# Performance work log

Hardware: AMD Instinct MI355X
Metric: run time of the kernel (lower is better)

The kernel has to match this reference:

```python
import jax, jax.numpy as jnp
import numpy as np

B, SX, TY = 256, 180, 160
D, DK, DV, H, DFF, V = 512, 64, 64, 8, 2048, 30
EPS = 1e-5


def _ln(x, g, b):
    m = jnp.mean(x, axis=-1, keepdims=True)
    v = jnp.mean(jnp.square(x - m), axis=-1, keepdims=True)
    return (x - m) / jnp.sqrt(v + EPS) * g + b


def _mha(q, kv, wq, wk, wv, pw, pb, masked):
    # per-head projections, vectorized over heads (source loops in Python)
    C = q.shape[-1]  # scale uses d_model (input dim), faithful to source
    Q = jnp.einsum('btd,hdk->bhtk', q, wq)
    K = jnp.einsum('bsd,hdk->bhsk', kv, wk)
    Vv = jnp.einsum('bsd,hdv->bhsv', kv, wv)
    W = jnp.einsum('bhtk,bhsk->bhts', Q, K) / (C ** 0.5)
    if masked:
        T = q.shape[1]
        tri = jnp.tril(jnp.ones((T, T), dtype=bool))
        W = jnp.where(tri, W, -jnp.inf)
    W = jax.nn.softmax(W, axis=-1)  # dropout is identity at rate 0 / eval
    out = jnp.einsum('bhts,bhsv->bthv', W, Vv)
    out = out.reshape(q.shape[0], q.shape[1], -1)  # concat heads -> [B,T,H*DV]
    return out @ pw + pb


def _attn_block(q, kv, wq, wk, wv, pw, pb, g, b, masked):
    res = q + _mha(q, kv, wq, wk, wv, pw, pb, masked)
    return _ln(res, g, b)


def _ff_block(x, w1, b1, w2, b2, g, b):
    h = jax.nn.relu(x @ w1 + b1) @ w2 + b2
    return _ln(x + h, g, b)


def setup_inputs() -> dict:
    key = jax.random.key(0)
    ks = iter(jax.random.split(key, 64))

    def n(shape, s=0.05):
        return jax.random.normal(next(ks), shape, jnp.float32) * s

    inp = {}
    inp['x'] = jax.random.normal(next(ks), (B, SX, 2), jnp.float32)
    inp['targets'] = jax.random.randint(next(ks), (B, TY + 1), 0, V, jnp.int32)
    inp['spec_w'] = n((2, D), 0.5)
    inp['spec_b'] = jnp.zeros((D,), jnp.float32)
    inp['pep_emb'] = n((V, D), 0.5)
    for p in ['enc_at', 'dec_sat', 'dec_cat']:
        inp[p + '_wq'] = n((H, D, DK))
        inp[p + '_wk'] = n((H, D, DK))
        inp[p + '_wv'] = n((H, D, DV))
        inp[p + '_pw'] = n((H * DV, D))
        inp[p + '_pb'] = jnp.zeros((D,), jnp.float32)
        inp[p + '_g'] = jnp.ones((D,), jnp.float32)
        inp[p + '_b'] = jnp.zeros((D,), jnp.float32)
    for p in ['enc_ff', 'dec_ff']:
        inp[p + '_w1'] = n((D, DFF))
        inp[p + '_b1'] = jnp.zeros((DFF,), jnp.float32)
        inp[p + '_w2'] = n((DFF, D))
        inp[p + '_b2'] = jnp.zeros((D,), jnp.float32)
        inp[p + '_g'] = jnp.ones((D,), jnp.float32)
        inp[p + '_b'] = jnp.zeros((D,), jnp.float32)
    inp['ll_w'] = n((D, V))
    inp['ll_b'] = jnp.zeros((V,), jnp.float32)
    return inp


def reference(x, targets, spec_w, spec_b, pep_emb,
              enc_at_wq, enc_at_wk, enc_at_wv, enc_at_pw, enc_at_pb, enc_at_g, enc_at_b,
              dec_sat_wq, dec_sat_wk, dec_sat_wv, dec_sat_pw, dec_sat_pb, dec_sat_g, dec_sat_b,
              dec_cat_wq, dec_cat_wk, dec_cat_wv, dec_cat_pw, dec_cat_pb, dec_cat_g, dec_cat_b,
              enc_ff_w1, enc_ff_b1, enc_ff_w2, enc_ff_b2, enc_ff_g, enc_ff_b,
              dec_ff_w1, dec_ff_b1, dec_ff_w2, dec_ff_b2, dec_ff_g, dec_ff_b,
              ll_w, ll_b):
    tgt = targets[:, :-1]
    xe = x @ spec_w + spec_b                      # spectrum embedding [B,SX,D]
    enc = _attn_block(xe, xe, enc_at_wq, enc_at_wk, enc_at_wv, enc_at_pw, enc_at_pb, enc_at_g, enc_at_b, False)
    enc = _ff_block(enc, enc_ff_w1, enc_ff_b1, enc_ff_w2, enc_ff_b2, enc_ff_g, enc_ff_b)
    de = pep_emb[tgt]                             # peptide embedding [B,TY,D]
    d1 = _attn_block(de, de, dec_sat_wq, dec_sat_wk, dec_sat_wv, dec_sat_pw, dec_sat_pb, dec_sat_g, dec_sat_b, True)
    d2 = _attn_block(d1, enc, dec_cat_wq, dec_cat_wk, dec_cat_wv, dec_cat_pw, dec_cat_pb, dec_cat_g, dec_cat_b, False)
    d3 = _ff_block(d2, dec_ff_w1, dec_ff_b1, dec_ff_w2, dec_ff_b2, dec_ff_g, dec_ff_b)
    return d3 @ ll_w + ll_b                       # logits [B,TY,V]
```

## Files before the change

### kernel.cpp

```cpp
#include <hip/hip_runtime.h>
#include <hip/hip_bf16.h>

typedef __hip_bfloat16 bf16;
typedef __attribute__((ext_vector_type(8))) short short8;
typedef __attribute__((ext_vector_type(4))) float f32x4;

#define BB   256
#define SXX  180
#define TYY  160
#define DD   512
#define DKK  64
#define HH   8
#define DFFF 2048
#define VV   30

#define NE (BB * SXX)
#define ND (BB * TYY)
#define N_IN 40

#ifndef __has_builtin
#define __has_builtin(x) 0
#endif

__global__ void k_detect(const unsigned short* __restrict__ probe, int* __restrict__ flag)
{
    if (threadIdx.x == 0 && blockIdx.x == 0)
        *flag = (probe[0] != 0x3F80) ? 1 : 0;
}

__device__ __forceinline__ float ldin(const void* src, long i, int f32)
{
    return f32 ? ((const float*)src)[i] : __bfloat162float(((const bf16*)src)[i]);
}

struct ImpD { const void* src; bf16* dst; int n; int K; int N; int mode; int blk0; int pad; };
struct ImpT { ImpD d[N_IN]; };

__global__ __launch_bounds__(256) void k_import_all(ImpT t, const int* __restrict__ flag)
{
    const int bid = blockIdx.x;
    int which = 0;
    #pragma unroll
    for (int k = 1; k < N_IN; ++k)
        if (bid >= t.d[k].blk0) which = k;
    ImpD d = t.d[which];
    if (d.mode == 3) return;
    long li = (long)(bid - d.blk0) * 256 + threadIdx.x;
    if (li >= d.n) return;
    int f32 = *flag;
    float v;
    if (d.mode == 0) {
        v = ldin(d.src, li, f32);
    } else if (d.mode == 1) {
        int nrow = (int)(li / d.K);
        int k    = (int)(li - (long)nrow * d.K);
        v = (nrow < d.N) ? ldin(d.src, (long)k * d.N + nrow, f32) : 0.f;
    } else {
        int n1 = (int)(li >> 9), dd = (int)(li & 511);
        v = ldin(d.src, (long)(n1 >> 6) * (DD * DKK) + (long)dd * DKK + (n1 & 63), f32);
    }
    d.dst[li] = __float2bfloat16(v);
}

__global__ __launch_bounds__(256) void k_embed_spec(
    const bf16* __restrict__ x, const bf16* __restrict__ w,
    const bf16* __restrict__ b, bf16* __restrict__ out)
{
    long i = (long)blockIdx.x * 256 + threadIdx.x;
    if (i >= (long)NE * DD) return;
    long tok = i >> 9;
    int  d   = (int)(i & 511);
    float x0 = __bfloat162float(x[tok * 2 + 0]);
    float x1 = __bfloat162float(x[tok * 2 + 1]);
    out[i] = __float2bfloat16(x0 * __bfloat162float(w[d])
                            + x1 * __bfloat162float(w[DD + d])
                            + __bfloat162float(b[d]));
}

__global__ __launch_bounds__(256) void k_gather(
    const int* __restrict__ tg, const bf16* __restrict__ emb, bf16* __restrict__ out)
{
    long tok = blockIdx.x;
    int  b   = (int)(tok / TYY);
    int  t   = (int)(tok - (long)b * TYY);
    int  idx = tg[(long)b * (TYY + 1) + t];
    const bf16* src = emb + (long)idx * DD;
    bf16*       dst = out + tok * DD;
    dst[threadIdx.x]       = src[threadIdx.x];
    dst[threadIdx.x + 256] = src[threadIdx.x + 256];
}

__device__ __forceinline__ void stage16(const bf16* g, bf16* l)
{
#if __has_builtin(__builtin_amdgcn_global_load_lds)
    __builtin_amdgcn_global_load_lds(
        (const __attribute__((address_space(1))) unsigned int*)g,
        (__attribute__((address_space(3))) unsigned int*)l, 16, 0, 0);
#else
    *(short8*)l = *(const short8*)g;
#endif
}

__global__ __launch_bounds__(256, 1) void k_mgemm(
    const bf16* __restrict__ A, const bf16* __restrict__ BT,
    const bf16* __restrict__ bias, const bf16* __restrict__ res,
    void* __restrict__ C,
    int M, int N, int K, int lda, int ldb, int ldc,
    int relu, const int* __restrict__ outf32)
{
    __shared__ __align__(16) bf16 sh[8192];
    bf16* As = sh;
    bf16* Bs = sh + 4096;

    const int tid  = threadIdx.x;
    const int lane = tid & 63;
    const int w    = tid >> 6;
    const int m0   = blockIdx.y * 128;
    const int n0   = blockIdx.x * 128;
    const int mw   = (w >> 1) * 64;
    const int nw   = (w & 1) * 64;

    f32x4 acc[4][4];
    #pragma unroll
    for (int i = 0; i < 4; ++i)
        #pragma unroll
        for (int j = 0; j < 4; ++j)
            acc[i][j] = (f32x4){0.f, 0.f, 0.f, 0.f};

    const int  sr = tid >> 2;
    const int  sk = (tid & 3) * 8;
    const bf16* Ag0 = A  + (size_t)(m0 + sr) * lda + sk;
    const bf16* Ag1 = Ag0 + (size_t)64 * lda;
    const bf16* Bg0 = BT + (size_t)(n0 + sr) * ldb + sk;
    const bf16* Bg1 = Bg0 + (size_t)64 * ldb;
    bf16* Al0 = As + sr * 32 + sk;
    bf16* Al1 = Al0 + 64 * 32;
    bf16* Bl0 = Bs + sr * 32 + sk;
    bf16* Bl1 = Bl0 + 64 * 32;

    const int lc = lane & 15, lq = lane >> 4;

    for (int k0 = 0; k0 < K; k0 += 32) {
        stage16(Ag0 + k0, Al0);
        stage16(Ag1 + k0, Al1);
        stage16(Bg0 + k0, Bl0);
        stage16(Bg1 + k0, Bl1);
        __syncthreads();

        short8 af[4], bfr[4];
        #pragma unroll
        for (int i = 0; i < 4; ++i)
            af[i] = *(const short8*)(As + (mw + i * 16 + lc) * 32 + lq * 8);
        #pragma unroll
        for (int j = 0; j < 4; ++j)
            bfr[j] = *(const short8*)(Bs + (nw + j * 16 + lc) * 32 + lq * 8);

        #pragma unroll
        for (int i = 0; i < 4; ++i)
            #pragma unroll
            for (int j = 0; j < 4; ++j)
                acc[i][j] = __builtin_amdgcn_mfma_f32_16x16x32_bf16(
                    af[i], bfr[j], acc[i][j], 0, 0, 0);

        __syncthreads();
    }

    const int f32o = (outf32 != nullptr) ? *outf32 : 0;

    if (!f32o && (N & 127) == 0) {
        float bv[4];
        #pragma unroll
        for (int j = 0; j < 4; ++j)
            bv[j] = bias ? __bfloat162float(bias[n0 + nw + j * 16 + lc]) : 0.f;
        bf16* ep = sh;
        #pragma unroll
        for (int i = 0; i < 4; ++i) {
            __syncthreads();
            #pragma unroll
            for (int j = 0; j < 4; ++j)
                #pragma unroll
                for (int r = 0; r < 4; ++r) {
                    float v = acc[i][j][r] + bv[j];
                    if (relu && v < 0.f) v = 0.f;
                    int lr = (w >> 1) * 16 + lq * 4 + r;
                    ep[lr * 136 + nw + j * 16 + lc] = __float2bfloat16(v);
                }
            __syncthreads();
            #pragma unroll
            for (int u = 0; u < 2; ++u) {
                int slot = tid + 256 * u;
                int lr   = slot >> 4;
                int cb   = (slot & 15) << 3;
                int gm   = m0 + 16 * i + ((lr & 16) ? (48 + lr) : lr);
                int gn   = n0 + cb;
                short8 val = *(short8*)(ep + lr * 136 + cb);
                if (res) {
                    short8 rv = *(const short8*)(res + (size_t)gm * ldc + gn);
                    #pragma unroll
                    for (int e = 0; e < 8; ++e) {
                        float s = __bfloat162float(((bf16*)&val)[e])
                                + __bfloat162float(((bf16*)&rv)[e]);
                        ((bf16*)&val)[e] = __float2bfloat16(s);
                    }
                }
                *(short8*)((bf16*)C + (size_t)gm * ldc + gn) = val;
            }
        }
    } else {
        #pragma unroll
        for (int j = 0; j < 4; ++j) {
            int gn = n0 + nw + j * 16 + lc;
            if (gn >= N) continue;
            float bvj = bias ? __bfloat162float(bias[gn]) : 0.f;
            #pragma unroll
            for (int i = 0; i < 4; ++i) {
                int gm = m0 + mw + i * 16 + lq * 4;
                #pragma unroll
                for (int r = 0; r < 4; ++r) {
                    float v = acc[i][j][r] + bvj;
                    if (relu && v < 0.f) v = 0.f;
                    size_t off = (size_t)(gm + r) * ldc + gn;
                    if (res) v += __bfloat162float(res[off]);
                    if (f32o) ((float*)C)[off] = v;
                    else      ((bf16*)C)[off]  = __float2bfloat16(v);
                }
            }
        }
    }
}

__global__ __launch_bounds__(256, 1) void k_fattn(
    const bf16* __restrict__ Q, const bf16* __restrict__ Kc,
    const bf16* __restrict__ Vt, bf16* __restrict__ O,
    int T, int S, int b_off, int causal, int ldv)
{
    __shared__ __align__(16) bf16 Pl[4 * 48 * 72];
    const int bl = blockIdx.x, h = blockIdx.y;
    const int tid = threadIdx.x, lane = tid & 63, w = tid >> 6;
    const int lc = lane & 15, lq = lane >> 4;
    const int wr0 = w * 48;
    const float scl = 0.044194173824159216f;

    short8 Qf[3][2];
    #pragma unroll
    for (int i = 0; i < 3; ++i) {
        int t = wr0 + 16 * i + lc;
        if (t >= T) t = T - 1;
        const bf16* qp = Q + ((size_t)(bl + b_off) * T + t) * DD + h * 64;
        #pragma unroll
        for (int kt = 0; kt < 2; ++kt)
            Qf[i][kt] = *(const short8*)(qp + kt * 32 + lq * 8);
    }

    float mrow[3][4], lrow[3][4];
    f32x4 oacc[3][4];
    #pragma unroll
    for (int i = 0; i < 3; ++i)
        #pragma unroll
        for (int r = 0; r < 4; ++r) { mrow[i][r] = -1e30f; lrow[i][r] = 0.f; }
    #pragma unroll
    for (int i = 0; i < 3; ++i)
        #pragma unroll
        for (int n = 0; n < 4; ++n)
            oacc[i][n] = (f32x4){0.f, 0.f, 0.f, 0.f};

    bf16* pw = Pl + w * 48 * 72;

    for (int c0 = 0; c0 < 192; c0 += 64) {
        if (causal && c0 > wr0 + 47) continue;

        short8 Kf[4][2];
        #pragma unroll
        for (int j = 0; j < 4; ++j) {
            int s = c0 + 16 * j + lc;
            if (s >= S) s = S - 1;
            const bf16* kp = Kc + ((size_t)bl * S + s) * DD + h * 64;
            #pragma unroll
            for (int kt = 0; kt < 2; ++kt)
                Kf[j][kt] = *(const short8*)(kp + kt * 32 + lq * 8);
        }

        f32x4 sa[3][4];
        #pragma unroll
        for (int i = 0; i < 3; ++i)
            #pragma unroll
            for (int j = 0; j < 4; ++j)
                sa[i][j] = (f32x4){0.f, 0.f, 0.f, 0.f};
        #pragma unroll
        for (int i = 0; i < 3; ++i)
            #pragma unroll
            for (int j = 0; j < 4; ++j)
                #pragma unroll
                for (int kt = 0; kt < 2; ++kt)
                    sa[i][j] = __builtin_amdgcn_mfma_f32_16x16x32_bf16(
                        Qf[i][kt], Kf[j][kt], sa[i][j], 0, 0, 0);

        #pragma unroll
        for (int i = 0; i < 3; ++i)
            #pragma unroll
            for (int j = 0; j < 4; ++j) {
                int col = c0 + 16 * j + lc;
                #pragma unroll
                for (int r = 0; r < 4; ++r) {
                    int row = wr0 + 16 * i + lq * 4 + r;
                    float v = sa[i][j][r] * scl;
                    if (col >= S || (causal && col > row)) v = -1e30f;
                    sa[i][j][r] = v;
                }
            }

        float corr[3][4];
        #pragma unroll
        for (int i = 0; i < 3; ++i)
            #pragma unroll
            for (int r = 0; r < 4; ++r) {
                float cm = fmaxf(fmaxf(sa[i][0][r], sa[i][1][r]),
                                 fmaxf(sa[i][2][r], sa[i][3][r]));
                cm = fmaxf(cm, __shfl_xor(cm, 1));
                cm = fmaxf(cm, __shfl_xor(cm, 2));
                cm = fmaxf(cm, __shfl_xor(cm, 4));
                cm = fmaxf(cm, __shfl_xor(cm, 8));
                float mn = fmaxf(mrow[i][r], cm);
                corr[i][r] = __expf(mrow[i][r] - mn);
                mrow[i][r] = mn;
            }
        #pragma unroll
        for (int i = 0; i < 3; ++i)
            #pragma unroll
            for (int j = 0; j < 4; ++j)
                #pragma unroll
                for (int r = 0; r < 4; ++r)
                    sa[i][j][r] = __expf(sa[i][j][r] - mrow[i][r]);
        #pragma unroll
        for (int i = 0; i < 3; ++i)
            #pragma unroll
            for (int r = 0; r < 4; ++r) {
                float sm = sa[i][0][r] + sa[i][1][r] + sa[i][2][r] + sa[i][3][r];
                sm += __shfl_xor(sm, 1);
                sm += __shfl_xor(sm, 2);
                sm += __shfl_xor(sm, 4);
                sm += __shfl_xor(sm, 8);
                lrow[i][r] = lrow[i][r] * corr[i][r] + sm;
            }

        #pragma unroll
        for (int i = 0; i < 3; ++i)
            #pragma unroll
            for (int j = 0; j < 4; ++j)
                #pragma unroll
                for (int r = 0; r < 4; ++r)
                    pw[(16 * i + lq * 4 + r) * 72 + 16 * j + lc] =
                        __float2bfloat16(sa[i][j][r]);

        short8 Pf[3][2], Vf[4][2];
        #pragma unroll
        for (int i = 0; i < 3; ++i)
            #pragma unroll
            for (int kt = 0; kt < 2; ++kt)
                Pf[i][kt] = *(const short8*)(pw + (16 * i + lc) * 72 + kt * 32 + lq * 8);
        #pragma unroll
        for (int n = 0; n < 4; ++n)
            #pragma unroll
            for (int kt = 0; kt < 2; ++kt)
                Vf[n][kt] = *(const short8*)(Vt + (size_t)(h * 64 + 16 * n + lc) * ldv
                                             + (size_t)bl * S + c0 + kt * 32 + lq * 8);

        #pragma unroll
        for (int i = 0; i < 3; ++i)
            #pragma unroll
            for (int n = 0; n < 4; ++n) {
                #pragma unroll
                for (int r = 0; r < 4; ++r)
                    oacc[i][n][r] *= corr[i][r];
                #pragma unroll
                for (int kt = 0; kt < 2; ++kt)
                    oacc[i][n] = __builtin_amdgcn_mfma_f32_16x16x32_bf16(
                        Pf[i][kt], Vf[n][kt], oacc[i][n], 0, 0, 0);
            }
    }

    #pragma unroll
    for (int i = 0; i < 3; ++i)
        #pragma unroll
        for (int r = 0; r < 4; ++r) {
            int t = wr0 + 16 * i + lq * 4 + r;
            if (t >= T) continue;
            float inv = 1.f / lrow[i][r];
            bf16* op = O + ((size_t)(bl + b_off) * T + t) * DD + h * 64;
            #pragma unroll
            for (int n = 0; n < 4; ++n)
                op[16 * n + lc] = __float2bfloat16(oacc[i][n][r] * inv);
        }
}

__global__ __launch_bounds__(256) void k_ln(
    const bf16* __restrict__ in, const bf16* __restrict__ g,
    const bf16* __restrict__ b, bf16* __restrict__ out)
{
    __shared__ float red[256];
    long long base = (long long)blockIdx.x * DD;
    int tid = threadIdx.x;
    float v0 = __bfloat162float(in[base + tid]);
    float v1 = __bfloat162float(in[base + 256 + tid]);

    red[tid] = v0 + v1; __syncthreads();
    for (int st = 128; st > 0; st >>= 1) {
        if (tid < st) red[tid] += red[tid + st];
        __syncthreads();
    }
    float mean = red[0] * (1.f / DD);
    __syncthreads();

    float d0 = v0 - mean, d1 = v1 - mean;
    red[tid] = d0 * d0 + d1 * d1; __syncthreads();
    for (int st = 128; st > 0; st >>= 1) {
        if (tid < st) red[tid] += red[tid + st];
        __syncthreads();
    }
    float rstd = rsqrtf(red[0] * (1.f / DD) + 1e-5f);

    out[base + tid] = __float2bfloat16(d0 * rstd * __bfloat162float(g[tid])
                                       + __bfloat162float(b[tid]));
    out[base + 256 + tid] = __float2bfloat16(d1 * rstd * __bfloat162float(g[tid + 256])
                                             + __bfloat162float(b[tid + 256]));
}

static inline void mgemm(hipStream_t s, const bf16* A, const bf16* BT, const bf16* bias,
                         const bf16* res, void* C, int M, int N, int K,
                         int lda, int ldb, int ldc, int relu, const int* outf32 = nullptr)
{
    dim3 grid((N + 127) / 128, M / 128);
    k_mgemm<<<grid, dim3(256), 0, s>>>(A, BT, bias, res, C, M, N, K, lda, ldb, ldc,
                                       relu, outf32);
}

extern "C" void kernel_launch(void* const* d_in, const int* in_sizes, int n_in,
                              void* d_out, int out_size, void* d_ws, size_t ws_size,
                              hipStream_t stream)
{
    char* base = (char*)d_ws;
    size_t o = 0;
    auto take = [&](size_t bytes) { size_t r = o; o += (bytes + 255) & ~(size_t)255; return r; };

    int* dflag = (int*)(base + take(256));
    k_detect<<<dim3(1), dim3(64), 0, stream>>>((const unsigned short*)d_in[10], dflag);

    ImpT tab;
    int blk = 0;
    const bf16* cv[N_IN];
    auto add_imp = [&](int i, int mode, int K, int N, int n_elems) {
        bf16* dst = (bf16*)(base + take((size_t)n_elems * 2));
        tab.d[i] = ImpD{d_in[i], dst, n_elems, K, N, mode, blk, 0};
        blk += (n_elems + 255) / 256;
        cv[i] = dst;
    };
    for (int i = 0; i < N_IN; ++i) {
        if (i == 1) { tab.d[i] = ImpD{nullptr, nullptr, 0, 0, 0, 3, blk, 0}; cv[i] = nullptr; continue; }
        bool qkv = (i == 5 || i == 6 || i == 7 || i == 12 || i == 13 || i == 14 ||
                    i == 19 || i == 20 || i == 21);
        if (qkv)                        add_imp(i, 2, 0, 0, DD * DD);
        else if (i == 8 || i == 15 || i == 22) add_imp(i, 1, DD, DD, DD * DD);
        else if (i == 26 || i == 32)    add_imp(i, 1, DD, DFFF, DFFF * DD);
        else if (i == 28 || i == 34)    add_imp(i, 1, DFFF, DD, DD * DFFF);
        else if (i == 38)               add_imp(i, 1, DD, VV, 128 * DD);
        else                            add_imp(i, 0, 0, 0, in_sizes[i]);
    }
    k_import_all<<<dim3(blk), dim3(256), 0, stream>>>(tab, dflag);

    const int* targets = (const int*)d_in[1];
    const bf16 *x = cv[0], *spec_w = cv[2], *spec_b = cv[3], *pep_emb = cv[4];
    const bf16 *eat_wq = cv[5],  *eat_wk = cv[6],  *eat_wvT = cv[7],  *eat_pw = cv[8],
               *eat_pb = cv[9],  *eat_g  = cv[10], *eat_b   = cv[11];
    const bf16 *sat_wq = cv[12], *sat_wk = cv[13], *sat_wvT = cv[14], *sat_pw = cv[15],
               *sat_pb = cv[16], *sat_g  = cv[17], *sat_b   = cv[18];
    const bf16 *cat_wq = cv[19], *cat_wk = cv[20], *cat_wvT = cv[21], *cat_pw = cv[22],
               *cat_pb = cv[23], *cat_g  = cv[24], *cat_b   = cv[25];
    const bf16 *eff_w1 = cv[26], *eff_b1 = cv[27], *eff_w2 = cv[28], *eff_b2 = cv[29],
               *eff_g  = cv[30], *eff_b  = cv[31];
    const bf16 *dff_w1 = cv[32], *dff_b1 = cv[33], *dff_w2 = cv[34], *dff_b2 = cv[35],
               *dff_g  = cv[36], *dff_b  = cv[37];
    const bf16 *ll_w = cv[38], *ll_b = cv[39];

    const size_t REG = (size_t)NE * DD * 2;
    bf16* A = (bf16*)(base + take(REG));
    bf16* B = (bf16*)(base + take(REG));
    bf16* C = (bf16*)(base + take(REG));
    bf16* D = (bf16*)(base + take(REG + 4096));
    bf16* D2 = D + (size_t)(NE / 2) * DD;

    k_embed_spec<<<dim3((NE * DD + 255) / 256), dim3(256), 0, stream>>>(x, spec_w, spec_b, A);

    mgemm(stream, A, eat_wq, nullptr, nullptr, B, NE, DD, DD, DD, DD, DD, 0);
    for (int hb = 0; hb < 2; ++hb) {
        const bf16* kv = A + (size_t)hb * (NE / 2) * DD;
        mgemm(stream, kv, eat_wk, nullptr, nullptr, D, NE / 2, DD, DD, DD, DD, DD, 0);
        mgemm(stream, eat_wvT, kv, nullptr, nullptr, D2, DD, NE / 2, DD, DD, DD, NE / 2, 0);
        k_fattn<<<dim3(BB / 2, HH), dim3(256), 0, stream>>>(
            B, D, D2, B, SXX, SXX, hb * (BB / 2), 0, NE / 2);
    }
    mgemm(stream, B, eat_pw, eat_pb, A, C, NE, DD, DD, DD, DD, DD, 0);
    k_ln<<<dim3(NE), dim3(256), 0, stream>>>(C, eat_g, eat_b, A);

    {
        const int CH = NE / 4;
        for (int c = 0; c < 4; ++c) {
            const bf16* Ain = A + (size_t)c * CH * DD;
            mgemm(stream, Ain, eff_w1, eff_b1, nullptr, B, CH, DFFF, DD, DD, DD, DFFF, 1);
            mgemm(stream, B, eff_w2, eff_b2, Ain, C + (size_t)c * CH * DD,
                  CH, DD, DFFF, DFFF, DFFF, DD, 0);
        }
        k_ln<<<dim3(NE), dim3(256), 0, stream>>>(C, eff_g, eff_b, C);
    }

    k_gather<<<dim3(ND), dim3(256), 0, stream>>>(targets, pep_emb, A);

    mgemm(stream, A, sat_wq, nullptr, nullptr, B, ND, DD, DD, DD, DD, DD, 0);
    for (int hb = 0; hb < 2; ++hb) {
        const bf16* kv = A + (size_t)hb * (ND / 2) * DD;
        mgemm(stream, kv, sat_wk, nullptr, nullptr, D, ND / 2, DD, DD, DD, DD, DD, 0);
        mgemm(stream, sat_wvT, kv, nullptr, nullptr, D2, DD, ND / 2, DD, DD, DD, ND / 2, 0);
        k_fattn<<<dim3(BB / 2, HH), dim3(256), 0, stream>>>(
            B, D, D2, B, TYY, TYY, hb * (BB / 2), 1, ND / 2);
    }
    mgemm(stream, B, sat_pw, sat_pb, A, D, ND, DD, DD, DD, DD, DD, 0);
    k_ln<<<dim3(ND), dim3(256), 0, stream>>>(D, sat_g, sat_b, A);

    mgemm(stream, A, cat_wq, nullptr, nullptr, B, ND, DD, DD, DD, DD, DD, 0);
    for (int hb = 0; hb < 2; ++hb) {
        const bf16* kv = C + (size_t)hb * (NE / 2) * DD;
        mgemm(stream, kv, cat_wk, nullptr, nullptr, D, NE / 2, DD, DD, DD, DD, DD, 0);
        mgemm(stream, cat_wvT, kv, nullptr, nullptr, D2, DD, NE / 2, DD, DD, DD, NE / 2, 0);
        k_fattn<<<dim3(BB / 2, HH), dim3(256), 0, stream>>>(
            B, D, D2, B, TYY, SXX, hb * (BB / 2), 0, NE / 2);
    }
    mgemm(stream, B, cat_pw, cat_pb, A, D, ND, DD, DD, DD, DD, DD, 0);
    k_ln<<<dim3(ND), dim3(256), 0, stream>>>(D, cat_g, cat_b, A);

    {
        const int CH = ND / 4;
        for (int c = 0; c < 4; ++c) {
            const bf16* Ain = A + (size_t)c * CH * DD;
            mgemm(stream, Ain, dff_w1, dff_b1, nullptr, B, CH, DFFF, DD, DD, DD, DFFF, 1);
            mgemm(stream, B, dff_w2, dff_b2, Ain, D + (size_t)c * CH * DD,
                  CH, DD, DFFF, DFFF, DFFF, DD, 0);
        }
        k_ln<<<dim3(ND), dim3(256), 0, stream>>>(D, dff_g, dff_b, D);
    }

    mgemm(stream, D, ll_w, ll_b, nullptr, d_out, ND, VV, DD, DD, DD, VV, 0, dflag);

    (void)in_sizes; (void)n_in; (void)out_size; (void)ws_size;
}
```

Baseline: 2.058 ms.

## Double-buffer GEMM LDS tiles and halve FFN chunk count

The GEMM main loop now keeps two LDS buffers. It prefetches the next K-slice with global_load_lds while MFMAs consume the current one, which drops one barrier per iteration. This targets the exposed global-load latency of the single-buffered loop, at the cost of doubling LDS to 32 KB per block. The FFN stages now run in two chunks instead of four, giving larger and fewer GEMM launches. To make room, the FFN hidden buffer is allowed to spill from B into the adjacent C region, and the attention scratch buffers are reassigned to match.

```diff
diff --git a/kernel.cpp b/kernel.cpp
--- a/kernel.cpp
+++ b/kernel.cpp
@@ -108,9 +108,7 @@
     int M, int N, int K, int lda, int ldb, int ldc,
     int relu, const int* __restrict__ outf32)
 {
-    __shared__ __align__(16) bf16 sh[8192];
-    bf16* As = sh;
-    bf16* Bs = sh + 4096;
+    __shared__ __align__(16) bf16 sh[16384];
 
     const int tid  = threadIdx.x;
     const int lane = tid & 63;
@@ -133,27 +131,33 @@
     const bf16* Ag1 = Ag0 + (size_t)64 * lda;
     const bf16* Bg0 = BT + (size_t)(n0 + sr) * ldb + sk;
     const bf16* Bg1 = Bg0 + (size_t)64 * ldb;
-    bf16* Al0 = As + sr * 32 + sk;
-    bf16* Al1 = Al0 + 64 * 32;
-    bf16* Bl0 = Bs + sr * 32 + sk;
-    bf16* Bl1 = Bl0 + 64 * 32;
+    const int lofs = sr * 32 + sk;
 
     const int lc = lane & 15, lq = lane >> 4;
 
+    stage16(Ag0, sh + lofs);
+    stage16(Ag1, sh + 2048 + lofs);
+    stage16(Bg0, sh + 4096 + lofs);
+    stage16(Bg1, sh + 6144 + lofs);
+
     for (int k0 = 0; k0 < K; k0 += 32) {
-        stage16(Ag0 + k0, Al0);
-        stage16(Ag1 + k0, Al1);
-        stage16(Bg0 + k0, Bl0);
-        stage16(Bg1 + k0, Bl1);
+        bf16* cb = sh + ((k0 >> 5) & 1) * 8192;
         __syncthreads();
+        if (k0 + 32 < K) {
+            bf16* nb = sh + ((~(k0 >> 5)) & 1) * 8192;
+            stage16(Ag0 + k0 + 32, nb + lofs);
+            stage16(Ag1 + k0 + 32, nb + 2048 + lofs);
+            stage16(Bg0 + k0 + 32, nb + 4096 + lofs);
+            stage16(Bg1 + k0 + 32, nb + 6144 + lofs);
+        }
 
         short8 af[4], bfr[4];
         #pragma unroll
         for (int i = 0; i < 4; ++i)
-            af[i] = *(const short8*)(As + (mw + i * 16 + lc) * 32 + lq * 8);
+            af[i] = *(const short8*)(cb + (mw + i * 16 + lc) * 32 + lq * 8);
         #pragma unroll
         for (int j = 0; j < 4; ++j)
-            bfr[j] = *(const short8*)(Bs + (nw + j * 16 + lc) * 32 + lq * 8);
+            bfr[j] = *(const short8*)(cb + 4096 + (nw + j * 16 + lc) * 32 + lq * 8);
 
         #pragma unroll
         for (int i = 0; i < 4; ++i)
@@ -161,8 +165,6 @@
             for (int j = 0; j < 4; ++j)
                 acc[i][j] = __builtin_amdgcn_mfma_f32_16x16x32_bf16(
                     af[i], bfr[j], acc[i][j], 0, 0, 0);
-
-        __syncthreads();
     }
 
     const int f32o = (outf32 != nullptr) ? *outf32 : 0;
@@ -190,10 +192,10 @@
             for (int u = 0; u < 2; ++u) {
                 int slot = tid + 256 * u;
                 int lr   = slot >> 4;
-                int cb   = (slot & 15) << 3;
+                int cb2  = (slot & 15) << 3;
                 int gm   = m0 + 16 * i + ((lr & 16) ? (48 + lr) : lr);
-                int gn   = n0 + cb;
-                short8 val = *(short8*)(ep + lr * 136 + cb);
+                int gn   = n0 + cb2;
+                short8 val = *(short8*)(ep + lr * 136 + cb2);
                 if (res) {
                     short8 rv = *(const short8*)(res + (size_t)gm * ldc + gn);
                     #pragma unroll
@@ -486,7 +488,8 @@
     bf16* B = (bf16*)(base + take(REG));
     bf16* C = (bf16*)(base + take(REG));
     bf16* D = (bf16*)(base + take(REG + 4096));
-    bf16* D2 = D + (size_t)(NE / 2) * DD;
+    bf16* D2  = D + (size_t)(NE / 2) * DD;
+    bf16* H   = B;
 
     k_embed_spec<<<dim3((NE * DD + 255) / 256), dim3(256), 0, stream>>>(x, spec_w, spec_b, A);
 
@@ -502,46 +505,48 @@
     k_ln<<<dim3(NE), dim3(256), 0, stream>>>(C, eat_g, eat_b, A);
 
     {
-        const int CH = NE / 4;
-        for (int c = 0; c < 4; ++c) {
+        const int CH = NE / 2;
+        for (int c = 0; c < 2; ++c) {
             const bf16* Ain = A + (size_t)c * CH * DD;
-            mgemm(stream, Ain, eff_w1, eff_b1, nullptr, B, CH, DFFF, DD, DD, DD, DFFF, 1);
-            mgemm(stream, B, eff_w2, eff_b2, Ain, C + (size_t)c * CH * DD,
+            mgemm(stream, Ain, eff_w1, eff_b1, nullptr, H, CH, DFFF, DD, DD, DD, DFFF, 1);
+            mgemm(stream, H, eff_w2, eff_b2, Ain, D + (size_t)c * CH * DD,
                   CH, DD, DFFF, DFFF, DFFF, DD, 0);
         }
-        k_ln<<<dim3(NE), dim3(256), 0, stream>>>(C, eff_g, eff_b, C);
+        k_ln<<<dim3(NE), dim3(256), 0, stream>>>(D, eff_g, eff_b, D);
     }
 
     k_gather<<<dim3(ND), dim3(256), 0, stream>>>(targets, pep_emb, A);
 
+    bf16* C2d = C + (size_t)(ND / 2) * DD;
     mgemm(stream, A, sat_wq, nullptr, nullptr, B, ND, DD, DD, DD, DD, DD, 0);
     for (int hb = 0; hb < 2; ++hb) {
         const bf16* kv = A + (size_t)hb * (ND / 2) * DD;
-        mgemm(stream, kv, sat_wk, nullptr, nullptr, D, ND / 2, DD, DD, DD, DD, DD, 0);
-        mgemm(stream, sat_wvT, kv, nullptr, nullptr, D2, DD, ND / 2, DD, DD, DD, ND / 2, 0);
+        mgemm(stream, kv, sat_wk, nullptr, nullptr, C, ND / 2, DD, DD, DD, DD, DD, 0);
+        mgemm(stream, sat_wvT, kv, nullptr, nullptr, C2d, DD, ND / 2, DD, DD, DD, ND / 2, 0);
         k_fattn<<<dim3(BB / 2, HH), dim3(256), 0, stream>>>(
-            B, D, D2, B, TYY, TYY, hb * (BB / 2), 1, ND / 2);
-    }
-    mgemm(stream, B, sat_pw, sat_pb, A, D, ND, DD, DD, DD, DD, DD, 0);
-    k_ln<<<dim3(ND), dim3(256), 0, stream>>>(D, sat_g, sat_b, A);
-
+            B, C, C2d, B, TYY, TYY, hb * (BB / 2), 1, ND / 2);
+    }
+    mgemm(stream, B, sat_pw, sat_pb, A, C, ND, DD, DD, DD, DD, DD, 0);
+    k_ln<<<dim3(ND), dim3(256), 0, stream>>>(C, sat_g, sat_b, A);
+
+    bf16* C2e = C + (size_t)(NE / 2) * DD;
     mgemm(stream, A, cat_wq, nullptr, nullptr, B, ND, DD, DD, DD, DD, DD, 0);
     for (int hb = 0; hb < 2; ++hb) {
-        const bf16* kv = C + (size_t)hb * (NE / 2) * DD;
-        mgemm(stream, kv, cat_wk, nullptr, nullptr, D, NE / 2, DD, DD, DD, DD, DD, 0);
-        mgemm(stream, cat_wvT, kv, nullptr, nullptr, D2, DD, NE / 2, DD, DD, DD, NE / 2, 0);
+        const bf16* kv = D + (size_t)hb * (NE / 2) * DD;
+        mgemm(stream, kv, cat_wk, nullptr, nullptr, C, NE / 2, DD, DD, DD, DD, DD, 0);
+        mgemm(stream, cat_wvT, kv, nullptr, nullptr, C2e, DD, NE / 2, DD, DD, DD, NE / 2, 0);
         k_fattn<<<dim3(BB / 2, HH), dim3(256), 0, stream>>>(
-            B, D, D2, B, TYY, SXX, hb * (BB / 2), 0, NE / 2);
-    }
-    mgemm(stream, B, cat_pw, cat_pb, A, D, ND, DD, DD, DD, DD, DD, 0);
-    k_ln<<<dim3(ND), dim3(256), 0, stream>>>(D, cat_g, cat_b, A);
+            B, C, C2e, B, TYY, SXX, hb * (BB / 2), 0, NE / 2);
+    }
+    mgemm(stream, B, cat_pw, cat_pb, A, C, ND, DD, DD, DD, DD, DD, 0);
+    k_ln<<<dim3(ND), dim3(256), 0, stream>>>(C, cat_g, cat_b, A);
 
     {
-        const int CH = ND / 4;
-        for (int c = 0; c < 4; ++c) {
+        const int CH = ND / 2;
+        for (int c = 0; c < 2; ++c) {
             const bf16* Ain = A + (size_t)c * CH * DD;
-            mgemm(stream, Ain, dff_w1, dff_b1, nullptr, B, CH, DFFF, DD, DD, DD, DFFF, 1);
-            mgemm(stream, B, dff_w2, dff_b2, Ain, D + (size_t)c * CH * DD,
+            mgemm(stream, Ain, dff_w1, dff_b1, nullptr, H, CH, DFFF, DD, DD, DD, DFFF, 1);
+            mgemm(stream, H, dff_w2, dff_b2, Ain, D + (size_t)c * CH * DD,
                   CH, DD, DFFF, DFFF, DFFF, DD, 0);
         }
         k_ln<<<dim3(ND), dim3(256), 0, stream>>>(D, dff_g, dff_b, D);
```

After: 1.760 ms. 1.17x faster.
